# Kernel tuning notes

Measured on AMD Instinct MI355X. Metric: run time of the kernel, lower is better.

The kernel has to match this reference:

```python
import jax, jax.numpy as jnp
import numpy as np

# NOTE: the original source omits the definitions of QSVT, quantum_lcu_block,
# QuantumSumBlock and KANLayer. We reconstruct the standard math these blocks
# implement in quantum-KAN papers/repos:
#   QSVT(x)            -> vector of Chebyshev polynomials T_1..T_D of the
#                         (squashed) input, the polynomial basis QSVT realizes.
#   quantum_lcu_block  -> linear combination of unitaries: weighted sum of the
#                         QSVT vector normalized by the LCU l1 weight norm.
#   QuantumSumBlock    -> learnable interference sum: mean_k sin(alpha_k * v).
#   KANLayer           -> Chebyshev-KAN layer: spline term (Chebyshev basis
#                         contracted with coeffs) + SiLU base branch + bias.
# Everything is fully vectorized over (B, F) instead of the original per-scalar
# Python loops.

B, F, DEG, C, KBASIS = 16384, 512, 8, 10, 8


def _cheb(x, K):
    """Chebyshev features T_1..T_K of x in (-1, 1): shape x.shape + (K,)."""
    t = jnp.arccos(jnp.clip(x, -1.0, 1.0))
    k = jnp.arange(1, K + 1, dtype=x.dtype)
    return jnp.cos(t[..., None] * k)


def setup_inputs() -> dict:
    key = jax.random.key(0)
    ks = jax.random.split(key, 6)
    return {
        "X": jax.random.normal(ks[0], (B, F), dtype=jnp.float32),
        # nn.Parameter(torch.rand(num_features, degree))
        "lcu_weights": jax.random.uniform(ks[1], (F, DEG), dtype=jnp.float32),
        # one QuantumSumBlock(degree) per feature -> (F, DEG) phases
        "sum_alpha": jax.random.normal(ks[2], (F, DEG), dtype=jnp.float32),
        # KANLayer params
        "kan_coeff": jax.random.normal(ks[3], (C, F, KBASIS), dtype=jnp.float32) * 0.1,
        "kan_base": jax.random.normal(ks[4], (C, F), dtype=jnp.float32) * 0.1,
        "kan_bias": jnp.zeros((C,), dtype=jnp.float32),
    }


def reference(X, lcu_weights, sum_alpha, kan_coeff, kan_base, kan_bias):
    # squash inputs into the open interval (-1, 1) for the Chebyshev/QSVT basis
    x = 0.99 * jnp.tanh(X)                                   # (B, F)
    # QSVT polynomial feature vector per scalar, batched: (B, F, DEG)
    qsvt = _cheb(x, lcu_weights.shape[1])
    # LCU block: weighted combination normalized by l1 norm of weights -> (B, F)
    lcu = jnp.einsum('bfd,fd->bf', qsvt, lcu_weights) / (
        jnp.sum(jnp.abs(lcu_weights), axis=-1) + 1e-8)
    # Quantum sum block: learnable sinusoidal interference sum -> (B, F)
    summed = jnp.mean(jnp.sin(lcu[..., None] * sum_alpha), axis=-1)
    # Chebyshev-KAN layer
    s = 0.99 * jnp.tanh(summed)
    phi = _cheb(s, kan_coeff.shape[2])                       # (B, F, KBASIS)
    logits = (jnp.einsum('bfk,cfk->bc', phi, kan_coeff)
              + jax.nn.silu(summed) @ kan_base.T
              + kan_bias)                                    # (B, C)
    return logits
```

## Files before the change

kernel.cpp:

```cpp
#include <hip/hip_runtime.h>

#define BATCH 16384
#define NF    512
#define DEG   8
#define NC    10
#define KB    8

#define SPLITF 8
#define FC     (NF / SPLITF)
#define RB     64
#define PITCH  68
#define NT     256
#define NWAVES 4

typedef __attribute__((ext_vector_type(8))) short bfrag;
typedef __attribute__((ext_vector_type(4))) float f32x4;

union frag_u { bfrag s; unsigned u[4]; };

__device__ __forceinline__ float fast_tanh(float x) {
    float e = __expf(2.0f * x);
    return 1.0f - 2.0f * __builtin_amdgcn_rcpf(e + 1.0f);
}
__device__ __forceinline__ float fast_sigmoid(float x) {
    return __builtin_amdgcn_rcpf(1.0f + __expf(-x));
}
__device__ __forceinline__ unsigned bfpack2(float lo, float hi) {
    unsigned ul = __builtin_bit_cast(unsigned, lo) + 0x8000u;
    unsigned uh = __builtin_bit_cast(unsigned, hi) + 0x8000u;
    return __builtin_amdgcn_perm(uh, ul, 0x07060302);
}
__device__ __forceinline__ bfrag cheb_frag(float s) {
    float T[KB];
    float tkm1 = 1.0f, tk = s;
    const float s2 = 2.0f * s;
#pragma unroll
    for (int k = 0; k < KB; ++k) {
        T[k] = tk;
        float tn = fmaf(s2, tk, -tkm1);
        tkm1 = tk; tk = tn;
    }
    frag_u f;
#pragma unroll
    for (int i = 0; i < 4; ++i) f.u[i] = bfpack2(T[2 * i], T[2 * i + 1]);
    return f.s;
}

__global__ __launch_bounds__(NT, 6) void qkan_kernel(
    const float* __restrict__ X,
    const float* __restrict__ lcu_w,
    const float* __restrict__ alpha,
    const float* __restrict__ coeff,
    const float* __restrict__ base,
    float* __restrict__ ws)
{
    __shared__ float s_mem[RB * PITCH];

    const int t      = threadIdx.x;
    const int rowblk = blockIdx.x >> 3;
    const int fsplit = blockIdx.x & (SPLITF - 1);
    const int row0   = rowblk * RB;
    const int fbase  = fsplit * FC;

    {
        const int f2   = t & 31;
        const int rsub = t >> 5;
        const int fA   = fbase + f2 * 2;

        float w[2][DEG], a[2][DEG], rden[2];
#pragma unroll
        for (int i = 0; i < 2; ++i) {
            const float4 w0 = *(const float4*)(lcu_w + (fA + i) * DEG);
            const float4 w1 = *(const float4*)(lcu_w + (fA + i) * DEG + 4);
            const float4 a0 = *(const float4*)(alpha + (fA + i) * DEG);
            const float4 a1 = *(const float4*)(alpha + (fA + i) * DEG + 4);
            w[i][0]=w0.x; w[i][1]=w0.y; w[i][2]=w0.z; w[i][3]=w0.w;
            w[i][4]=w1.x; w[i][5]=w1.y; w[i][6]=w1.z; w[i][7]=w1.w;
            a[i][0]=a0.x; a[i][1]=a0.y; a[i][2]=a0.z; a[i][3]=a0.w;
            a[i][4]=a1.x; a[i][5]=a1.y; a[i][6]=a1.z; a[i][7]=a1.w;
            float den = 1e-8f;
#pragma unroll
            for (int d = 0; d < DEG; ++d) den += fabsf(w[i][d]);
            rden[i] = __builtin_amdgcn_rcpf(den);
        }

#pragma unroll
        for (int it = 0; it < RB / 8; ++it) {
            const int r = rsub + it * 8;
            const float2 xv = *(const float2*)(X + (row0 + r) * NF + fA);
            float xs[2] = {xv.x, xv.y};
            float sums[2];
#pragma unroll
            for (int i = 0; i < 2; ++i) {
                const float x  = 0.99f * fast_tanh(xs[i]);
                const float x2 = 2.0f * x;
                float tkm1 = 1.0f, tk = x, num = 0.0f;
#pragma unroll
                for (int d = 0; d < DEG; ++d) {
                    num = fmaf(w[i][d], tk, num);
                    float tn = fmaf(x2, tk, -tkm1);
                    tkm1 = tk; tk = tn;
                }
                const float lcu = num * rden[i];
                float ss = 0.0f;
#pragma unroll
                for (int d = 0; d < DEG; ++d)
                    ss += __sinf(lcu * a[i][d]);
                sums[i] = 0.125f * ss;
            }
            *(float2*)(&s_mem[r * PITCH + f2 * 2]) = make_float2(sums[0], sums[1]);
        }
    }
    __syncthreads();

    const int lane = t & 63;
    const int wave = __builtin_amdgcn_readfirstlane(t >> 6);
    const int n    = lane & 15;
    const int q    = lane >> 4;
    const bool nv  = (n < NC);
    const int  ncl = nv ? n : (NC - 1);
    const int rl   = wave * 16 + n;

    f32x4 acc = {0.f, 0.f, 0.f, 0.f};

#pragma unroll 4
    for (int kt = 0; kt < 16; ++kt) {
        const float* p = coeff + (ncl * NF + fbase + kt * 4 + q) * KB;
        const float4 c0 = *(const float4*)p;
        const float4 c1 = *(const float4*)(p + 4);
        frag_u fb;
        fb.u[0] = bfpack2(c0.x, c0.y); fb.u[1] = bfpack2(c0.z, c0.w);
        fb.u[2] = bfpack2(c1.x, c1.y); fb.u[3] = bfpack2(c1.z, c1.w);

        const float sm = s_mem[rl * PITCH + kt * 4 + q];
        const bfrag av = cheb_frag(0.99f * fast_tanh(sm));
        acc = __builtin_amdgcn_mfma_f32_16x16x32_bf16(av, fb.s, acc, 0, 0, 0);
    }

#pragma unroll
    for (int kt2 = 0; kt2 < 2; ++kt2) {
        const float* p = base + ncl * NF + fbase + kt2 * 32 + q * 8;
        const float4 b0 = *(const float4*)p;
        const float4 b1 = *(const float4*)(p + 4);
        frag_u fb;
        fb.u[0] = bfpack2(b0.x, b0.y); fb.u[1] = bfpack2(b0.z, b0.w);
        fb.u[2] = bfpack2(b1.x, b1.y); fb.u[3] = bfpack2(b1.z, b1.w);

        const int off = kt2 * 32 + q * 8;
        const float4 v0 = *(const float4*)(&s_mem[rl * PITCH + off]);
        const float4 v1 = *(const float4*)(&s_mem[rl * PITCH + off + 4]);
        float v[8] = {v0.x, v0.y, v0.z, v0.w, v1.x, v1.y, v1.z, v1.w};
        float sl[8];
#pragma unroll
        for (int j = 0; j < 8; ++j)
            sl[j] = v[j] * fast_sigmoid(v[j]);
        frag_u fa;
        fa.u[0] = bfpack2(sl[0], sl[1]); fa.u[1] = bfpack2(sl[2], sl[3]);
        fa.u[2] = bfpack2(sl[4], sl[5]); fa.u[3] = bfpack2(sl[6], sl[7]);
        acc = __builtin_amdgcn_mfma_f32_16x16x32_bf16(fa.s, fb.s, acc, 0, 0, 0);
    }

    if (nv) {
        float* wsp = ws + (size_t)fsplit * (BATCH * NC);
#pragma unroll
        for (int i = 0; i < 4; ++i)
            wsp[(row0 + wave * 16 + q * 4 + i) * NC + n] = acc[i];
    }
}

__global__ __launch_bounds__(256) void reduce_kernel(
    const float* __restrict__ ws, const float* __restrict__ bias,
    float* __restrict__ out)
{
    const int idx = blockIdx.x * 256 + threadIdx.x;
    if (idx < BATCH * NC) {
        const int c = idx % NC;
        float v = bias[c];
#pragma unroll
        for (int s = 0; s < SPLITF; ++s)
            v += ws[(size_t)s * (BATCH * NC) + idx];
        out[idx] = v;
    }
}

extern "C" void kernel_launch(void* const* d_in, const int* in_sizes, int n_in,
                              void* d_out, int out_size, void* d_ws, size_t ws_size,
                              hipStream_t stream) {
    const float* X      = (const float*)d_in[0];
    const float* lcu_w  = (const float*)d_in[1];
    const float* alpha  = (const float*)d_in[2];
    const float* coeff  = (const float*)d_in[3];
    const float* base   = (const float*)d_in[4];
    const float* bias   = (const float*)d_in[5];
    float* out = (float*)d_out;
    float* ws  = (float*)d_ws;

    qkan_kernel<<<(BATCH / RB) * SPLITF, NT, 0, stream>>>(X, lcu_w, alpha, coeff, base, ws);
    reduce_kernel<<<(BATCH * NC + 255) / 256, 256, 0, stream>>>(ws, bias, out);
}
```

Measured before the change: 108.6 us.

## Pre-pack KAN weights to bf16 and vectorize transcendental math with packed float2

Adds a prep kernel that converts coeff and base weights to bf16 once per launch, so the main kernel loads ready-made MFMA B-fragments instead of converting fp32 on every tile. The elementwise math (tanh, Chebyshev recurrences, sin via the hardware sin with pre-scaled phases, SiLU) is rewritten on float2 vectors so it can use packed FMA. The Chebyshev-KAN loop now handles two k-tiles per iteration into two independent accumulators to expose more MFMA ILP. The cost is an extra kernel launch and workspace space for the packed weights, plus a small accuracy shift from the hardware sin.

Result: faster. 100.4 us (-7.6%).

```diff
diff --git a/kernel.cpp b/kernel.cpp
--- a/kernel.cpp
+++ b/kernel.cpp
@@ -11,47 +11,68 @@
 #define RB     64
 #define PITCH  68
 #define NT     256
-#define NWAVES 4
-
+
+#define CBN (NC * NF * KB)
+#define BBN (NC * NF)
+#define WS_PART (SPLITF * BATCH * NC)
+
+#define INV2PI 0.15915494309189535f
+#define LOG2E  1.4426950408889634f
+
+typedef __attribute__((ext_vector_type(2))) float v2f;
 typedef __attribute__((ext_vector_type(8))) short bfrag;
 typedef __attribute__((ext_vector_type(4))) float f32x4;
 
 union frag_u { bfrag s; unsigned u[4]; };
 
-__device__ __forceinline__ float fast_tanh(float x) {
-    float e = __expf(2.0f * x);
-    return 1.0f - 2.0f * __builtin_amdgcn_rcpf(e + 1.0f);
-}
-__device__ __forceinline__ float fast_sigmoid(float x) {
-    return __builtin_amdgcn_rcpf(1.0f + __expf(-x));
+__device__ __forceinline__ v2f v2fma(v2f a, v2f b, v2f c) {
+    return __builtin_elementwise_fma(a, b, c);
+}
+__device__ __forceinline__ v2f v2exp(v2f x) {
+    v2f a = x * LOG2E;
+    v2f r; r.x = __builtin_amdgcn_exp2f(a.x); r.y = __builtin_amdgcn_exp2f(a.y);
+    return r;
+}
+__device__ __forceinline__ v2f v2rcp(v2f x) {
+    v2f r; r.x = __builtin_amdgcn_rcpf(x.x); r.y = __builtin_amdgcn_rcpf(x.y);
+    return r;
+}
+__device__ __forceinline__ v2f v2sin2pi(v2f x) {
+    v2f r; r.x = __builtin_amdgcn_sinf(x.x); r.y = __builtin_amdgcn_sinf(x.y);
+    return r;
+}
+__device__ __forceinline__ v2f v2tanh99(v2f x) {
+    v2f e = v2exp(x + x);
+    v2f r = v2rcp(e + 1.0f);
+    return v2fma(r, (v2f)(-1.98f), (v2f)(0.99f));
+}
+__device__ __forceinline__ v2f v2silu(v2f v) {
+    v2f e = v2exp(-v);
+    v2f r = v2rcp(e + 1.0f);
+    return v * r;
 }
 __device__ __forceinline__ unsigned bfpack2(float lo, float hi) {
     unsigned ul = __builtin_bit_cast(unsigned, lo) + 0x8000u;
     unsigned uh = __builtin_bit_cast(unsigned, hi) + 0x8000u;
     return __builtin_amdgcn_perm(uh, ul, 0x07060302);
 }
-__device__ __forceinline__ bfrag cheb_frag(float s) {
-    float T[KB];
-    float tkm1 = 1.0f, tk = s;
-    const float s2 = 2.0f * s;
-#pragma unroll
-    for (int k = 0; k < KB; ++k) {
-        T[k] = tk;
-        float tn = fmaf(s2, tk, -tkm1);
-        tkm1 = tk; tk = tn;
-    }
-    frag_u f;
-#pragma unroll
-    for (int i = 0; i < 4; ++i) f.u[i] = bfpack2(T[2 * i], T[2 * i + 1]);
-    return f.s;
+
+__global__ __launch_bounds__(256) void prep_kernel(
+    const float* __restrict__ coeff, const float* __restrict__ base,
+    unsigned short* __restrict__ pk)
+{
+    const int i = blockIdx.x * 256 + threadIdx.x;
+    if (i < CBN)
+        pk[i] = (unsigned short)((__builtin_bit_cast(unsigned, coeff[i]) + 0x8000u) >> 16);
+    else if (i < CBN + BBN)
+        pk[i] = (unsigned short)((__builtin_bit_cast(unsigned, base[i - CBN]) + 0x8000u) >> 16);
 }
 
 __global__ __launch_bounds__(NT, 6) void qkan_kernel(
     const float* __restrict__ X,
     const float* __restrict__ lcu_w,
     const float* __restrict__ alpha,
-    const float* __restrict__ coeff,
-    const float* __restrict__ base,
+    const unsigned short* __restrict__ pk,
     float* __restrict__ ws)
 {
     __shared__ float s_mem[RB * PITCH];
@@ -67,48 +88,50 @@
         const int rsub = t >> 5;
         const int fA   = fbase + f2 * 2;
 
-        float w[2][DEG], a[2][DEG], rden[2];
+        float wa[2][DEG], aa[2][DEG], den[2];
 #pragma unroll
         for (int i = 0; i < 2; ++i) {
             const float4 w0 = *(const float4*)(lcu_w + (fA + i) * DEG);
             const float4 w1 = *(const float4*)(lcu_w + (fA + i) * DEG + 4);
             const float4 a0 = *(const float4*)(alpha + (fA + i) * DEG);
             const float4 a1 = *(const float4*)(alpha + (fA + i) * DEG + 4);
-            w[i][0]=w0.x; w[i][1]=w0.y; w[i][2]=w0.z; w[i][3]=w0.w;
-            w[i][4]=w1.x; w[i][5]=w1.y; w[i][6]=w1.z; w[i][7]=w1.w;
-            a[i][0]=a0.x; a[i][1]=a0.y; a[i][2]=a0.z; a[i][3]=a0.w;
-            a[i][4]=a1.x; a[i][5]=a1.y; a[i][6]=a1.z; a[i][7]=a1.w;
-            float den = 1e-8f;
-#pragma unroll
-            for (int d = 0; d < DEG; ++d) den += fabsf(w[i][d]);
-            rden[i] = __builtin_amdgcn_rcpf(den);
-        }
+            wa[i][0]=w0.x; wa[i][1]=w0.y; wa[i][2]=w0.z; wa[i][3]=w0.w;
+            wa[i][4]=w1.x; wa[i][5]=w1.y; wa[i][6]=w1.z; wa[i][7]=w1.w;
+            aa[i][0]=a0.x; aa[i][1]=a0.y; aa[i][2]=a0.z; aa[i][3]=a0.w;
+            aa[i][4]=a1.x; aa[i][5]=a1.y; aa[i][6]=a1.z; aa[i][7]=a1.w;
+            float d = 1e-8f;
+#pragma unroll
+            for (int k = 0; k < DEG; ++k) d += fabsf(wa[i][k]);
+            den[i] = d;
+        }
+        v2f W[DEG], A2[DEG];
+#pragma unroll
+        for (int d = 0; d < DEG; ++d) {
+            W[d]  = (v2f){wa[0][d], wa[1][d]};
+            A2[d] = (v2f){aa[0][d] * INV2PI, aa[1][d] * INV2PI};
+        }
+        const v2f rden = (v2f){__builtin_amdgcn_rcpf(den[0]),
+                               __builtin_amdgcn_rcpf(den[1])};
 
 #pragma unroll
         for (int it = 0; it < RB / 8; ++it) {
             const int r = rsub + it * 8;
-            const float2 xv = *(const float2*)(X + (row0 + r) * NF + fA);
-            float xs[2] = {xv.x, xv.y};
-            float sums[2];
-#pragma unroll
-            for (int i = 0; i < 2; ++i) {
-                const float x  = 0.99f * fast_tanh(xs[i]);
-                const float x2 = 2.0f * x;
-                float tkm1 = 1.0f, tk = x, num = 0.0f;
-#pragma unroll
-                for (int d = 0; d < DEG; ++d) {
-                    num = fmaf(w[i][d], tk, num);
-                    float tn = fmaf(x2, tk, -tkm1);
-                    tkm1 = tk; tk = tn;
-                }
-                const float lcu = num * rden[i];
-                float ss = 0.0f;
-#pragma unroll
-                for (int d = 0; d < DEG; ++d)
-                    ss += __sinf(lcu * a[i][d]);
-                sums[i] = 0.125f * ss;
+            const v2f xv = *(const v2f*)(X + (row0 + r) * NF + fA);
+            const v2f x  = v2tanh99(xv);
+            const v2f x2 = x + x;
+            v2f tkm1 = (v2f){1.0f, 1.0f}, tk = x, num = (v2f){0.0f, 0.0f};
+#pragma unroll
+            for (int d = 0; d < DEG; ++d) {
+                num = v2fma(W[d], tk, num);
+                v2f tn = v2fma(x2, tk, -tkm1);
+                tkm1 = tk; tk = tn;
             }
-            *(float2*)(&s_mem[r * PITCH + f2 * 2]) = make_float2(sums[0], sums[1]);
+            const v2f lcu = num * rden;
+            v2f ss = (v2f){0.0f, 0.0f};
+#pragma unroll
+            for (int d = 0; d < DEG; ++d)
+                ss += v2sin2pi(lcu * A2[d]);
+            *(v2f*)(&s_mem[r * PITCH + f2 * 2]) = ss * 0.125f;
         }
     }
     __syncthreads();
@@ -121,46 +144,60 @@
     const int  ncl = nv ? n : (NC - 1);
     const int rl   = wave * 16 + n;
 
-    f32x4 acc = {0.f, 0.f, 0.f, 0.f};
+    const unsigned short* cb = pk;
+    const unsigned short* bb = pk + CBN;
+    const unsigned short* cbase = cb + (ncl * NF + fbase) * KB;
+
+    f32x4 acc0 = {0.f, 0.f, 0.f, 0.f};
+    f32x4 acc1 = {0.f, 0.f, 0.f, 0.f};
 
 #pragma unroll 4
-    for (int kt = 0; kt < 16; ++kt) {
-        const float* p = coeff + (ncl * NF + fbase + kt * 4 + q) * KB;
-        const float4 c0 = *(const float4*)p;
-        const float4 c1 = *(const float4*)(p + 4);
-        frag_u fb;
-        fb.u[0] = bfpack2(c0.x, c0.y); fb.u[1] = bfpack2(c0.z, c0.w);
-        fb.u[2] = bfpack2(c1.x, c1.y); fb.u[3] = bfpack2(c1.z, c1.w);
-
-        const float sm = s_mem[rl * PITCH + kt * 4 + q];
-        const bfrag av = cheb_frag(0.99f * fast_tanh(sm));
-        acc = __builtin_amdgcn_mfma_f32_16x16x32_bf16(av, fb.s, acc, 0, 0, 0);
+    for (int kp = 0; kp < 8; ++kp) {
+        const bfrag b0 = *(const bfrag*)(cbase + (kp * 8 + q) * KB);
+        const bfrag b1 = *(const bfrag*)(cbase + (kp * 8 + 4 + q) * KB);
+
+        const float sA = s_mem[rl * PITCH + kp * 8 + q];
+        const float sB = s_mem[rl * PITCH + kp * 8 + 4 + q];
+        const v2f s  = v2tanh99((v2f){sA, sB});
+        const v2f s2 = s + s;
+        v2f T[KB];
+        {
+            v2f tkm1 = (v2f){1.0f, 1.0f}, tk = s;
+#pragma unroll
+            for (int k = 0; k < KB; ++k) {
+                T[k] = tk;
+                v2f tn = v2fma(s2, tk, -tkm1);
+                tkm1 = tk; tk = tn;
+            }
+        }
+        frag_u fa0, fa1;
+#pragma unroll
+        for (int i = 0; i < 4; ++i) {
+            fa0.u[i] = bfpack2(T[2 * i].x, T[2 * i + 1].x);
+            fa1.u[i] = bfpack2(T[2 * i].y, T[2 * i + 1].y);
+        }
+        acc0 = __builtin_amdgcn_mfma_f32_16x16x32_bf16(fa0.s, b0, acc0, 0, 0, 0);
+        acc1 = __builtin_amdgcn_mfma_f32_16x16x32_bf16(fa1.s, b1, acc1, 0, 0, 0);
     }
 
 #pragma unroll
     for (int kt2 = 0; kt2 < 2; ++kt2) {
-        const float* p = base + ncl * NF + fbase + kt2 * 32 + q * 8;
-        const float4 b0 = *(const float4*)p;
-        const float4 b1 = *(const float4*)(p + 4);
-        frag_u fb;
-        fb.u[0] = bfpack2(b0.x, b0.y); fb.u[1] = bfpack2(b0.z, b0.w);
-        fb.u[2] = bfpack2(b1.x, b1.y); fb.u[3] = bfpack2(b1.z, b1.w);
-
+        const bfrag b = *(const bfrag*)(bb + ncl * NF + fbase + kt2 * 32 + q * 8);
         const int off = kt2 * 32 + q * 8;
         const float4 v0 = *(const float4*)(&s_mem[rl * PITCH + off]);
         const float4 v1 = *(const float4*)(&s_mem[rl * PITCH + off + 4]);
-        float v[8] = {v0.x, v0.y, v0.z, v0.w, v1.x, v1.y, v1.z, v1.w};
-        float sl[8];
-#pragma unroll
-        for (int j = 0; j < 8; ++j)
-            sl[j] = v[j] * fast_sigmoid(v[j]);
+        v2f vv[4] = {{v0.x, v0.y}, {v0.z, v0.w}, {v1.x, v1.y}, {v1.z, v1.w}};
         frag_u fa;
-        fa.u[0] = bfpack2(sl[0], sl[1]); fa.u[1] = bfpack2(sl[2], sl[3]);
-        fa.u[2] = bfpack2(sl[4], sl[5]); fa.u[3] = bfpack2(sl[6], sl[7]);
-        acc = __builtin_amdgcn_mfma_f32_16x16x32_bf16(fa.s, fb.s, acc, 0, 0, 0);
+#pragma unroll
+        for (int g = 0; g < 4; ++g) {
+            const v2f sl = v2silu(vv[g]);
+            fa.u[g] = bfpack2(sl.x, sl.y);
+        }
+        acc0 = __builtin_amdgcn_mfma_f32_16x16x32_bf16(fa.s, b, acc0, 0, 0, 0);
     }
 
     if (nv) {
+        const f32x4 acc = acc0 + acc1;
         float* wsp = ws + (size_t)fsplit * (BATCH * NC);
 #pragma unroll
         for (int i = 0; i < 4; ++i)
@@ -194,7 +231,9 @@
     const float* bias   = (const float*)d_in[5];
     float* out = (float*)d_out;
     float* ws  = (float*)d_ws;
-
-    qkan_kernel<<<(BATCH / RB) * SPLITF, NT, 0, stream>>>(X, lcu_w, alpha, coeff, base, ws);
+    unsigned short* pk = (unsigned short*)(ws + WS_PART);
+
+    prep_kernel<<<(CBN + BBN + 255) / 256, 256, 0, stream>>>(coeff, base, pk);
+    qkan_kernel<<<(BATCH / RB) * SPLITF, NT, 0, stream>>>(X, lcu_w, alpha, pk, ws);
     reduce_kernel<<<(BATCH * NC + 255) / 256, 256, 0, stream>>>(ws, bias, out);
 }
```
